# Kernel tuning notes

Hardware: AMD Instinct MI355X
Metric: run time of the kernel (lower is better)

Reference implementation:

```python
import jax, jax.numpy as jnp
import numpy as np

N, M, FIN, K, NNZ = 16, 20000, 64, 4, 320000


def setup_inputs() -> dict:
    key = jax.random.key(0)
    k1, k2, k3, k4 = jax.random.split(key, 4)
    x = jax.random.normal(k1, (N, M, FIN), dtype=jnp.float32)
    L_vals = jax.random.normal(k2, (K, NNZ), dtype=jnp.float32)
    L_rows = jax.random.randint(k3, (K, NNZ), 0, M, dtype=jnp.int32)
    L_cols = jax.random.randint(k4, (K, NNZ), 0, M, dtype=jnp.int32)
    return {"x": x, "L_vals": L_vals, "L_rows": L_rows, "L_cols": L_cols}


def reference(x, L_vals, L_rows, L_cols):
    n, m, fin = x.shape
    kk = L_vals.shape[0]
    # x0: [M, Fin*N]  (transpose + reshape as in the original call())
    x0 = jnp.transpose(x, (1, 2, 0)).reshape(m, fin * n)

    def spmm_plus_x0(vals, rows, cols):
        # sparse [M,M] @ dense [M, Fin*N] via gather + segment-sum, then + x0
        contrib = vals[:, None] * x0[cols]            # [nnz, Fin*N]
        y = jax.ops.segment_sum(contrib, rows, num_segments=m)
        return y + x0

    x_con = jax.vmap(spmm_plus_x0)(L_vals, L_rows, L_cols)  # [K, M, Fin*N]
    out = x_con.reshape(kk, m, fin, n)
    out = jnp.transpose(out, (3, 1, 2, 0)).reshape(n, m, fin * kk)
    return jax.nn.relu(out)
```

## Files before the change

### kernel.cpp

```cpp
#include <hip/hip_runtime.h>

#define N_    16
#define M_    20000
#define FIN_  64
#define K_    4
#define NNZ_  320000
#define KM_   (K_ * M_)
#define KNNZ_ (K_ * NNZ_)
#define CAP_  64


#define XT_BYTES   ((size_t)M_ * FIN_ * N_ * 2)
#define CNT_BYTES  ((size_t)KM_ * 4)
#define SLOT_BYTES ((size_t)KM_ * CAP_ * 4)
#define WS_A (XT_BYTES + CNT_BYTES + SLOT_BYTES)
#define WS_B (CNT_BYTES + SLOT_BYTES)

__device__ __forceinline__ unsigned bf16bits(float v) {
    unsigned u = __float_as_uint(v);
    return (u + 0x7FFFu + ((u >> 16) & 1u)) & 0xFFFF0000u;
}

__global__ __launch_bounds__(256) void transpose_kernel(const float* __restrict__ x,
                                                        uint4* __restrict__ xt4) {
    int wid = threadIdx.x >> 6, f = threadIdx.x & 63;
    int m = blockIdx.x * 4 + wid;
    unsigned h[16];
    #pragma unroll
    for (int n = 0; n < N_; ++n)
        h[n] = bf16bits(x[((size_t)n * M_ + m) * FIN_ + f]) >> 16;
    uint4 A, B;
    A.x = h[0]  | (h[1]  << 16); A.y = h[2]  | (h[3]  << 16);
    A.z = h[4]  | (h[5]  << 16); A.w = h[6]  | (h[7]  << 16);
    B.x = h[8]  | (h[9]  << 16); B.y = h[10] | (h[11] << 16);
    B.z = h[12] | (h[13] << 16); B.w = h[14] | (h[15] << 16);
    size_t base = ((size_t)m * 64 + f) * 2;
    xt4[base] = A; xt4[base + 1] = B;
}

__global__ void zero_cnt_kernel(int* __restrict__ cnt) {
    int i = blockIdx.x * blockDim.x + threadIdx.x;
    if (i < KM_) cnt[i] = 0;
}

__global__ void bin_kernel(const float* __restrict__ vals,
                           const int*   __restrict__ rows,
                           const int*   __restrict__ cols,
                           int*      __restrict__ cnt,
                           unsigned* __restrict__ slots) {
    int idx = blockIdx.x * blockDim.x + threadIdx.x;
    if (idx >= KNNZ_) return;
    int k = idx / NNZ_;
    int b = k * M_ + rows[idx];
    int rank = atomicAdd(&cnt[b], 1);
    if (rank < CAP_)
        slots[(size_t)b * CAP_ + rank] = bf16bits(vals[idx]) | (unsigned)cols[idx];
}

__device__ __forceinline__ void fma16(float* a, float v, uint4 A, uint4 B) {
    a[0]  += v * __uint_as_float(A.x << 16);
    a[1]  += v * __uint_as_float(A.x & 0xFFFF0000u);
    a[2]  += v * __uint_as_float(A.y << 16);
    a[3]  += v * __uint_as_float(A.y & 0xFFFF0000u);
    a[4]  += v * __uint_as_float(A.z << 16);
    a[5]  += v * __uint_as_float(A.z & 0xFFFF0000u);
    a[6]  += v * __uint_as_float(A.w << 16);
    a[7]  += v * __uint_as_float(A.w & 0xFFFF0000u);
    a[8]  += v * __uint_as_float(B.x << 16);
    a[9]  += v * __uint_as_float(B.x & 0xFFFF0000u);
    a[10] += v * __uint_as_float(B.y << 16);
    a[11] += v * __uint_as_float(B.y & 0xFFFF0000u);
    a[12] += v * __uint_as_float(B.z << 16);
    a[13] += v * __uint_as_float(B.z & 0xFFFF0000u);
    a[14] += v * __uint_as_float(B.w << 16);
    a[15] += v * __uint_as_float(B.w & 0xFFFF0000u);
}

__global__ __launch_bounds__(256) void gather_bf16_kernel(const char* __restrict__ xtb,
                                                          const int* __restrict__ cnt,
                                                          const unsigned* __restrict__ slots,
                                                          float4* __restrict__ out4) {
    int wid = threadIdx.x >> 6;
    int f   = threadIdx.x & 63;
    int m   = blockIdx.x * 4 + wid;
    size_t lofs = (size_t)f * 2;

    float acc[K_][N_];
    {
        const uint4* pm = (const uint4*)(xtb + ((size_t)m << 11)) + lofs;
        uint4 A = pm[0], Bv = pm[1];
        float xv[16];
        xv[0]=__uint_as_float(A.x<<16);  xv[1]=__uint_as_float(A.x&0xFFFF0000u);
        xv[2]=__uint_as_float(A.y<<16);  xv[3]=__uint_as_float(A.y&0xFFFF0000u);
        xv[4]=__uint_as_float(A.z<<16);  xv[5]=__uint_as_float(A.z&0xFFFF0000u);
        xv[6]=__uint_as_float(A.w<<16);  xv[7]=__uint_as_float(A.w&0xFFFF0000u);
        xv[8]=__uint_as_float(Bv.x<<16); xv[9]=__uint_as_float(Bv.x&0xFFFF0000u);
        xv[10]=__uint_as_float(Bv.y<<16);xv[11]=__uint_as_float(Bv.y&0xFFFF0000u);
        xv[12]=__uint_as_float(Bv.z<<16);xv[13]=__uint_as_float(Bv.z&0xFFFF0000u);
        xv[14]=__uint_as_float(Bv.w<<16);xv[15]=__uint_as_float(Bv.w&0xFFFF0000u);
        #pragma unroll
        for (int k = 0; k < K_; ++k)
            #pragma unroll
            for (int n = 0; n < N_; ++n) acc[k][n] = xv[n];
    }

    #pragma unroll
    for (int k = 0; k < K_; ++k) {
        int b  = k * M_ + m;
        int cn = cnt[b];
        if (cn > CAP_) cn = CAP_;
        unsigned sl = slots[(size_t)b * CAP_ + f];
        for (int g = 0; g < cn; g += 4) {
            int s0 = (g + 0 < cn) ? __shfl((int)sl, g + 0, 64) : 0;
            int s1 = (g + 1 < cn) ? __shfl((int)sl, g + 1, 64) : 0;
            int s2 = (g + 2 < cn) ? __shfl((int)sl, g + 2, 64) : 0;
            int s3 = (g + 3 < cn) ? __shfl((int)sl, g + 3, 64) : 0;
            const uint4* p0 = (const uint4*)(xtb + (((size_t)((unsigned)s0 & 0xFFFFu)) << 11)) + lofs;
            const uint4* p1 = (const uint4*)(xtb + (((size_t)((unsigned)s1 & 0xFFFFu)) << 11)) + lofs;
            const uint4* p2 = (const uint4*)(xtb + (((size_t)((unsigned)s2 & 0xFFFFu)) << 11)) + lofs;
            const uint4* p3 = (const uint4*)(xtb + (((size_t)((unsigned)s3 & 0xFFFFu)) << 11)) + lofs;
            uint4 A0 = p0[0], B0 = p0[1];
            uint4 A1 = p1[0], B1 = p1[1];
            uint4 A2 = p2[0], B2 = p2[1];
            uint4 A3 = p3[0], B3 = p3[1];
            float v0 = __uint_as_float((unsigned)s0 & 0xFFFF0000u);
            float v1 = __uint_as_float((unsigned)s1 & 0xFFFF0000u);
            float v2 = __uint_as_float((unsigned)s2 & 0xFFFF0000u);
            float v3 = __uint_as_float((unsigned)s3 & 0xFFFF0000u);
            fma16(acc[k], v0, A0, B0);
            fma16(acc[k], v1, A1, B1);
            fma16(acc[k], v2, A2, B2);
            fma16(acc[k], v3, A3, B3);
        }
    }

    #pragma unroll
    for (int n = 0; n < N_; ++n) {
        float4 w;
        w.x = fmaxf(acc[0][n], 0.0f);
        w.y = fmaxf(acc[1][n], 0.0f);
        w.z = fmaxf(acc[2][n], 0.0f);
        w.w = fmaxf(acc[3][n], 0.0f);
        out4[((size_t)n * M_ + m) * FIN_ + f] = w;
    }
}

__global__ __launch_bounds__(256) void gather_f32_kernel(const float* __restrict__ x,
                                                         const int* __restrict__ cnt,
                                                         const unsigned* __restrict__ slots,
                                                         float4* __restrict__ out4) {
    int wid = threadIdx.x >> 6;
    int f   = threadIdx.x & 63;
    int m   = blockIdx.x * 4 + wid;

    float acc[K_][N_];
    #pragma unroll
    for (int n = 0; n < N_; ++n) {
        float xv = x[((size_t)n * M_ + m) * FIN_ + f];
        #pragma unroll
        for (int k = 0; k < K_; ++k) acc[k][n] = xv;
    }

    #pragma unroll
    for (int k = 0; k < K_; ++k) {
        int b  = k * M_ + m;
        int cn = cnt[b];
        if (cn > CAP_) cn = CAP_;
        unsigned sl = slots[(size_t)b * CAP_ + f];
        for (int j = 0; j < cn; ++j) {
            int s = __shfl((int)sl, j, 64);
            float v = __uint_as_float((unsigned)s & 0xFFFF0000u);
            int   c = (int)((unsigned)s & 0xFFFFu);
            const float* xp = x + (size_t)c * FIN_ + f;
            #pragma unroll
            for (int n = 0; n < N_; ++n)
                acc[k][n] += v * xp[(size_t)n * (M_ * FIN_)];
        }
    }

    #pragma unroll
    for (int n = 0; n < N_; ++n) {
        float4 w;
        w.x = fmaxf(acc[0][n], 0.0f);
        w.y = fmaxf(acc[1][n], 0.0f);
        w.z = fmaxf(acc[2][n], 0.0f);
        w.w = fmaxf(acc[3][n], 0.0f);
        out4[((size_t)n * M_ + m) * FIN_ + f] = w;
    }
}

__global__ void init_out_kernel(const float* __restrict__ x, float* __restrict__ out) {
    int i = blockIdx.x * blockDim.x + threadIdx.x;
    const int tot = N_ * M_ * FIN_;
    if (i < tot) {
        float v = x[i];
        reinterpret_cast<float4*>(out)[i] = make_float4(v, v, v, v);
    }
}

__global__ void scatter_kernel(const float* __restrict__ x,
                               const float* __restrict__ vals,
                               const int*   __restrict__ rows,
                               const int*   __restrict__ cols,
                               float* __restrict__ out) {
    long long idx = (long long)blockIdx.x * blockDim.x + threadIdx.x;
    int f  = (int)(idx & 63);
    int ea = (int)(idx >> 6);
    if (ea >= KNNZ_) return;
    int k = ea / NNZ_;
    float v = vals[ea];
    int r = rows[ea];
    int c = cols[ea];
    const float* xp = x   + (size_t)c * FIN_ + f;
    float*       op = out + ((size_t)r * FIN_ + f) * K_ + k;
    #pragma unroll
    for (int n = 0; n < N_; ++n)
        atomicAdd(op + (size_t)n * (M_ * FIN_ * K_), v * xp[(size_t)n * (M_ * FIN_)]);
}

__global__ void relu_kernel(float* __restrict__ out) {
    int i = blockIdx.x * blockDim.x + threadIdx.x;
    const int tot4 = (N_ * M_ * FIN_ * K_) / 4;
    if (i < tot4) {
        float4 v = reinterpret_cast<float4*>(out)[i];
        v.x = fmaxf(v.x, 0.0f); v.y = fmaxf(v.y, 0.0f);
        v.z = fmaxf(v.z, 0.0f); v.w = fmaxf(v.w, 0.0f);
        reinterpret_cast<float4*>(out)[i] = v;
    }
}

extern "C" void kernel_launch(void* const* d_in, const int* in_sizes, int n_in,
                              void* d_out, int out_size, void* d_ws, size_t ws_size,
                              hipStream_t stream) {
    const float* x    = (const float*)d_in[0];
    const float* vals = (const float*)d_in[1];
    const int*   rows = (const int*)d_in[2];
    const int*   cols = (const int*)d_in[3];
    float*       out  = (float*)d_out;
    char*        ws   = (char*)d_ws;

    if (ws_size >= WS_A) {
        char*     xtb   = ws;
        int*      cnt   = (int*)(ws + XT_BYTES);
        unsigned* slots = (unsigned*)(ws + XT_BYTES + CNT_BYTES);

        transpose_kernel<<<M_ / 4, 256, 0, stream>>>(x, (uint4*)xtb);
        zero_cnt_kernel<<<(KM_ + 255) / 256, 256, 0, stream>>>(cnt);
        bin_kernel<<<(KNNZ_ + 255) / 256, 256, 0, stream>>>(vals, rows, cols, cnt, slots);
        gather_bf16_kernel<<<M_ / 4, 256, 0, stream>>>(xtb, cnt, slots, (float4*)out);
    } else if (ws_size >= WS_B) {
        int*      cnt   = (int*)ws;
        unsigned* slots = (unsigned*)(ws + CNT_BYTES);

        zero_cnt_kernel<<<(KM_ + 255) / 256, 256, 0, stream>>>(cnt);
        bin_kernel<<<(KNNZ_ + 255) / 256, 256, 0, stream>>>(vals, rows, cols, cnt, slots);
        gather_f32_kernel<<<M_ / 4, 256, 0, stream>>>(x, cnt, slots, (float4*)out);
    } else {
        init_out_kernel<<<(N_ * M_ * FIN_ + 255) / 256, 256, 0, stream>>>(x, out);
        {
            long long tot = (long long)KNNZ_ * 64;
            scatter_kernel<<<(int)((tot + 255) / 256), 256, 0, stream>>>(x, vals, rows, cols, out);
        }
        relu_kernel<<<(N_ * M_ * FIN_ * K_ / 4 + 255) / 256, 256, 0, stream>>>(out);
    }
}
```

Before: 490.6 us.

## Split batch halves across waves with planar bf16 layout and fuse count zeroing

Changes the transposed bf16 layout so each row stores batch halves in two contiguous 64-entry planes, and makes the gather kernel assign one wave per (row, batch half). Each lane then holds 8 accumulators per k instead of 16, and the grid doubles. The inner loop now issues 8 independent 16-byte gathers per iteration. Count zeroing is folded into the transpose kernel to drop one launch. The slot list is now read and shuffled twice per row, once per half, in exchange for lower register pressure and more memory-level parallelism.

```diff
diff --git a/kernel.cpp b/kernel.cpp
--- a/kernel.cpp
+++ b/kernel.cpp
@@ -22,7 +22,11 @@
 }
 
 __global__ __launch_bounds__(256) void transpose_kernel(const float* __restrict__ x,
-                                                        uint4* __restrict__ xt4) {
+                                                        uint4* __restrict__ xt4,
+                                                        int* __restrict__ cnt) {
+    int gtid = blockIdx.x * 256 + threadIdx.x;
+    if (gtid < KM_) cnt[gtid] = 0;
+
     int wid = threadIdx.x >> 6, f = threadIdx.x & 63;
     int m = blockIdx.x * 4 + wid;
     unsigned h[16];
@@ -34,13 +38,8 @@
     A.z = h[4]  | (h[5]  << 16); A.w = h[6]  | (h[7]  << 16);
     B.x = h[8]  | (h[9]  << 16); B.y = h[10] | (h[11] << 16);
     B.z = h[12] | (h[13] << 16); B.w = h[14] | (h[15] << 16);
-    size_t base = ((size_t)m * 64 + f) * 2;
-    xt4[base] = A; xt4[base + 1] = B;
-}
-
-__global__ void zero_cnt_kernel(int* __restrict__ cnt) {
-    int i = blockIdx.x * blockDim.x + threadIdx.x;
-    if (i < KM_) cnt[i] = 0;
+    xt4[m * 128 + f]      = A;
+    xt4[m * 128 + 64 + f] = B;
 }
 
 __global__ void bin_kernel(const float* __restrict__ vals,
@@ -57,51 +56,39 @@
         slots[(size_t)b * CAP_ + rank] = bf16bits(vals[idx]) | (unsigned)cols[idx];
 }
 
-__device__ __forceinline__ void fma16(float* a, float v, uint4 A, uint4 B) {
-    a[0]  += v * __uint_as_float(A.x << 16);
-    a[1]  += v * __uint_as_float(A.x & 0xFFFF0000u);
-    a[2]  += v * __uint_as_float(A.y << 16);
-    a[3]  += v * __uint_as_float(A.y & 0xFFFF0000u);
-    a[4]  += v * __uint_as_float(A.z << 16);
-    a[5]  += v * __uint_as_float(A.z & 0xFFFF0000u);
-    a[6]  += v * __uint_as_float(A.w << 16);
-    a[7]  += v * __uint_as_float(A.w & 0xFFFF0000u);
-    a[8]  += v * __uint_as_float(B.x << 16);
-    a[9]  += v * __uint_as_float(B.x & 0xFFFF0000u);
-    a[10] += v * __uint_as_float(B.y << 16);
-    a[11] += v * __uint_as_float(B.y & 0xFFFF0000u);
-    a[12] += v * __uint_as_float(B.z << 16);
-    a[13] += v * __uint_as_float(B.z & 0xFFFF0000u);
-    a[14] += v * __uint_as_float(B.w << 16);
-    a[15] += v * __uint_as_float(B.w & 0xFFFF0000u);
-}
-
-__global__ __launch_bounds__(256) void gather_bf16_kernel(const char* __restrict__ xtb,
+__device__ __forceinline__ void fma8(float* a, float v, uint4 U) {
+    a[0] += v * __uint_as_float(U.x << 16);
+    a[1] += v * __uint_as_float(U.x & 0xFFFF0000u);
+    a[2] += v * __uint_as_float(U.y << 16);
+    a[3] += v * __uint_as_float(U.y & 0xFFFF0000u);
+    a[4] += v * __uint_as_float(U.z << 16);
+    a[5] += v * __uint_as_float(U.z & 0xFFFF0000u);
+    a[6] += v * __uint_as_float(U.w << 16);
+    a[7] += v * __uint_as_float(U.w & 0xFFFF0000u);
+}
+
+__global__ __launch_bounds__(256) void gather_bf16_kernel(const uint4* __restrict__ xt4,
                                                           const int* __restrict__ cnt,
                                                           const unsigned* __restrict__ slots,
                                                           float4* __restrict__ out4) {
     int wid = threadIdx.x >> 6;
     int f   = threadIdx.x & 63;
-    int m   = blockIdx.x * 4 + wid;
-    size_t lofs = (size_t)f * 2;
-
-    float acc[K_][N_];
+    int m   = blockIdx.x * 2 + (wid >> 1);
+    int hh  = wid & 1;
+    int hofs = hh * 64 + f;
+
+    float acc[K_][8];
     {
-        const uint4* pm = (const uint4*)(xtb + ((size_t)m << 11)) + lofs;
-        uint4 A = pm[0], Bv = pm[1];
-        float xv[16];
-        xv[0]=__uint_as_float(A.x<<16);  xv[1]=__uint_as_float(A.x&0xFFFF0000u);
-        xv[2]=__uint_as_float(A.y<<16);  xv[3]=__uint_as_float(A.y&0xFFFF0000u);
-        xv[4]=__uint_as_float(A.z<<16);  xv[5]=__uint_as_float(A.z&0xFFFF0000u);
-        xv[6]=__uint_as_float(A.w<<16);  xv[7]=__uint_as_float(A.w&0xFFFF0000u);
-        xv[8]=__uint_as_float(Bv.x<<16); xv[9]=__uint_as_float(Bv.x&0xFFFF0000u);
-        xv[10]=__uint_as_float(Bv.y<<16);xv[11]=__uint_as_float(Bv.y&0xFFFF0000u);
-        xv[12]=__uint_as_float(Bv.z<<16);xv[13]=__uint_as_float(Bv.z&0xFFFF0000u);
-        xv[14]=__uint_as_float(Bv.w<<16);xv[15]=__uint_as_float(Bv.w&0xFFFF0000u);
+        uint4 X = xt4[m * 128 + hofs];
+        float xv[8];
+        xv[0]=__uint_as_float(X.x<<16); xv[1]=__uint_as_float(X.x&0xFFFF0000u);
+        xv[2]=__uint_as_float(X.y<<16); xv[3]=__uint_as_float(X.y&0xFFFF0000u);
+        xv[4]=__uint_as_float(X.z<<16); xv[5]=__uint_as_float(X.z&0xFFFF0000u);
+        xv[6]=__uint_as_float(X.w<<16); xv[7]=__uint_as_float(X.w&0xFFFF0000u);
         #pragma unroll
         for (int k = 0; k < K_; ++k)
             #pragma unroll
-            for (int n = 0; n < N_; ++n) acc[k][n] = xv[n];
+            for (int j = 0; j < 8; ++j) acc[k][j] = xv[j];
     }
 
     #pragma unroll
@@ -110,37 +97,33 @@
         int cn = cnt[b];
         if (cn > CAP_) cn = CAP_;
         unsigned sl = slots[(size_t)b * CAP_ + f];
-        for (int g = 0; g < cn; g += 4) {
-            int s0 = (g + 0 < cn) ? __shfl((int)sl, g + 0, 64) : 0;
-            int s1 = (g + 1 < cn) ? __shfl((int)sl, g + 1, 64) : 0;
-            int s2 = (g + 2 < cn) ? __shfl((int)sl, g + 2, 64) : 0;
-            int s3 = (g + 3 < cn) ? __shfl((int)sl, g + 3, 64) : 0;
-            const uint4* p0 = (const uint4*)(xtb + (((size_t)((unsigned)s0 & 0xFFFFu)) << 11)) + lofs;
-            const uint4* p1 = (const uint4*)(xtb + (((size_t)((unsigned)s1 & 0xFFFFu)) << 11)) + lofs;
-            const uint4* p2 = (const uint4*)(xtb + (((size_t)((unsigned)s2 & 0xFFFFu)) << 11)) + lofs;
-            const uint4* p3 = (const uint4*)(xtb + (((size_t)((unsigned)s3 & 0xFFFFu)) << 11)) + lofs;
-            uint4 A0 = p0[0], B0 = p0[1];
-            uint4 A1 = p1[0], B1 = p1[1];
-            uint4 A2 = p2[0], B2 = p2[1];
-            uint4 A3 = p3[0], B3 = p3[1];
-            float v0 = __uint_as_float((unsigned)s0 & 0xFFFF0000u);
-            float v1 = __uint_as_float((unsigned)s1 & 0xFFFF0000u);
-            float v2 = __uint_as_float((unsigned)s2 & 0xFFFF0000u);
-            float v3 = __uint_as_float((unsigned)s3 & 0xFFFF0000u);
-            fma16(acc[k], v0, A0, B0);
-            fma16(acc[k], v1, A1, B1);
-            fma16(acc[k], v2, A2, B2);
-            fma16(acc[k], v3, A3, B3);
+        for (int g = 0; g < cn; g += 8) {
+            int s[8];
+            uint4 u[8];
+            #pragma unroll
+            for (int i = 0; i < 8; ++i)
+                s[i] = (g + i < cn) ? __shfl((int)sl, g + i, 64) : 0;
+            #pragma unroll
+            for (int i = 0; i < 8; ++i) {
+                int c = (int)((unsigned)s[i] & 0xFFFFu);
+                u[i] = xt4[c * 128 + hofs];
+            }
+            #pragma unroll
+            for (int i = 0; i < 8; ++i) {
+                float v = __uint_as_float((unsigned)s[i] & 0xFFFF0000u);
+                fma8(acc[k], v, u[i]);
+            }
         }
     }
 
     #pragma unroll
-    for (int n = 0; n < N_; ++n) {
+    for (int j = 0; j < 8; ++j) {
+        int n = hh * 8 + j;
         float4 w;
-        w.x = fmaxf(acc[0][n], 0.0f);
-        w.y = fmaxf(acc[1][n], 0.0f);
-        w.z = fmaxf(acc[2][n], 0.0f);
-        w.w = fmaxf(acc[3][n], 0.0f);
+        w.x = fmaxf(acc[0][j], 0.0f);
+        w.y = fmaxf(acc[1][j], 0.0f);
+        w.z = fmaxf(acc[2][j], 0.0f);
+        w.w = fmaxf(acc[3][j], 0.0f);
         out4[((size_t)n * M_ + m) * FIN_ + f] = w;
     }
 }
@@ -187,6 +170,11 @@
         w.w = fmaxf(acc[3][n], 0.0f);
         out4[((size_t)n * M_ + m) * FIN_ + f] = w;
     }
+}
+
+__global__ void zero_cnt_kernel(int* __restrict__ cnt) {
+    int i = blockIdx.x * blockDim.x + threadIdx.x;
+    if (i < KM_) cnt[i] = 0;
 }
 
 __global__ void init_out_kernel(const float* __restrict__ x, float* __restrict__ out) {
@@ -240,14 +228,13 @@
     char*        ws   = (char*)d_ws;
 
     if (ws_size >= WS_A) {
-        char*     xtb   = ws;
+        uint4*    xt4   = (uint4*)ws;
         int*      cnt   = (int*)(ws + XT_BYTES);
         unsigned* slots = (unsigned*)(ws + XT_BYTES + CNT_BYTES);
 
-        transpose_kernel<<<M_ / 4, 256, 0, stream>>>(x, (uint4*)xtb);
-        zero_cnt_kernel<<<(KM_ + 255) / 256, 256, 0, stream>>>(cnt);
+        transpose_kernel<<<M_ / 4, 256, 0, stream>>>(x, xt4, cnt);
         bin_kernel<<<(KNNZ_ + 255) / 256, 256, 0, stream>>>(vals, rows, cols, cnt, slots);
-        gather_bf16_kernel<<<M_ / 4, 256, 0, stream>>>(xtb, cnt, slots, (float4*)out);
+        gather_bf16_kernel<<<M_ / 2, 256, 0, stream>>>(xt4, cnt, slots, (float4*)out);
     } else if (ws_size >= WS_B) {
         int*      cnt   = (int*)ws;
         unsigned* slots = (unsigned*)(ws + CNT_BYTES);
```

New measurement: 485.7 us. No clear change (-1.0%).
